# Kernel tuning notes

Hardware: AMD Instinct MI355X
Metric: run time of the kernel (lower is better)

Reference implementation:

```python
import jax, jax.numpy as jnp
import numpy as np

DIM = 4096
N_HEADS = 32
N_KV = 8
HEAD_DIM = DIM // N_HEADS  # 128
R = N_HEADS // N_KV        # 4 query heads per kv head
B, T = 2, 2048


def setup_inputs() -> dict:
    key = jax.random.key(0)
    kx, kq, kkv, ko = jax.random.split(key, 4)
    scale = 0.02
    return {
        "x": jax.random.normal(kx, (B, T, DIM), dtype=jnp.float32),
        "Wq": jax.random.normal(kq, (DIM, DIM), dtype=jnp.float32) * scale,
        "Wkv": jax.random.normal(kkv, (2 * N_KV * HEAD_DIM, DIM), dtype=jnp.float32) * scale,
        "Wo": jax.random.normal(ko, (DIM, DIM), dtype=jnp.float32) * scale,
    }


def reference(x, Wq, Wkv, Wo):
    Bs, Ts, C = x.shape
    # projections (torch Linear: y = x @ W.T)
    q = (x @ Wq.T).reshape(Bs, Ts, N_HEADS, HEAD_DIM).transpose(0, 2, 1, 3)  # [B,H,T,hd]
    kv = x @ Wkv.T                                                            # [B,T,2*KV*hd]
    k, v = jnp.split(kv, 2, axis=-1)
    k = k.reshape(Bs, Ts, N_KV, HEAD_DIM).transpose(0, 2, 1, 3)  # [B,KV,T,hd]
    v = v.reshape(Bs, Ts, N_KV, HEAD_DIM).transpose(0, 2, 1, 3)  # [B,KV,T,hd]
    # grouped query heads: head h = g*R + r matches repeat_interleave(R, dim=1)
    qg = q.reshape(Bs, N_KV, R, Ts, HEAD_DIM)                    # [B,KV,R,T,hd]
    inv_scale = 1.0 / np.sqrt(HEAD_DIM).astype(np.float32)
    scores = jnp.einsum("bgrtd,bgsd->bgrts", qg, k) * inv_scale  # [B,KV,R,T,T]
    causal = jnp.tril(jnp.ones((Ts, Ts), dtype=bool))
    scores = jnp.where(causal, scores, jnp.finfo(scores.dtype).min)
    attn = jax.nn.softmax(scores, axis=-1)
    o = jnp.einsum("bgrts,bgsd->bgrtd", attn, v)                 # [B,KV,R,T,hd]
    o = o.reshape(Bs, N_HEADS, Ts, HEAD_DIM).transpose(0, 2, 1, 3).reshape(Bs, Ts, C)
    return o @ Wo.T
```

## Files before the change

### kernel.cpp

```cpp
#include <hip/hip_runtime.h>
#include <hip/hip_bf16.h>
#include <cstdint>
#include <type_traits>

#define DIM    4096
#define NHEADS 32
#define NKVH   8
#define HD     128
#define BATCH  2
#define SEQ    2048
#define MROWS  (BATCH*SEQ)
#define NQKV   6144
#define KOFF   4096
#define VOFF   5120

typedef __attribute__((ext_vector_type(8))) __bf16 bf16x8;
typedef __attribute__((ext_vector_type(4))) float  f32x4;

#define QSCALE 0.1275174338f

__device__ __forceinline__ void gl_lds16(const __bf16* g, __bf16* l) {
    __builtin_amdgcn_global_load_lds(
        (const __attribute__((address_space(1))) void*)g,
        (__attribute__((address_space(3))) void*)l, 16, 0, 0);
}

__global__ void cast_f32_bf16(const float* __restrict__ s, __bf16* __restrict__ d, int n8) {
    int i = blockIdx.x * 256 + threadIdx.x;
    if (i >= n8) return;
    float4 a = ((const float4*)s)[2*i];
    float4 b = ((const float4*)s)[2*i+1];
    bf16x8 v;
    v[0]=(__bf16)a.x; v[1]=(__bf16)a.y; v[2]=(__bf16)a.z; v[3]=(__bf16)a.w;
    v[4]=(__bf16)b.x; v[5]=(__bf16)b.y; v[6]=(__bf16)b.z; v[7]=(__bf16)b.w;
    ((bf16x8*)d)[i] = v;
}

template<typename OutT>
__global__ __launch_bounds__(256)
void gemm_bt(const __bf16* __restrict__ A, const __bf16* __restrict__ Bm,
             OutT* __restrict__ C, int M, int N, int K,
             float scale, int scale_cols)
{
    __shared__ __bf16 As[128*64];
    __shared__ __bf16 Bs[128*64];
    const int tid  = threadIdx.x;
    const int lane = tid & 63;
    const int w    = tid >> 6;
    const int quad = lane >> 4;
    const int l16  = lane & 15;
    const int m0   = blockIdx.y * 128;
    const int n0   = blockIdx.x * 128;
    const int wm   = (w & 1) * 64;
    const int wn   = (w >> 1) * 64;

    const __bf16* Ab = A  + (size_t)m0 * K;
    const __bf16* Bb = Bm + (size_t)n0 * K;

    f32x4 acc[4][4] = {};

    for (int k0 = 0; k0 < K; k0 += 64) {
        __syncthreads();
        #pragma unroll
        for (int r = 0; r < 4; ++r) {
            int chunk = r*256 + tid;
            int row = chunk >> 3, c8 = chunk & 7;
            int c8s = c8 ^ (row & 7);
            gl_lds16(Ab + (size_t)row*K + k0 + c8s*8, As + chunk*8);
            gl_lds16(Bb + (size_t)row*K + k0 + c8s*8, Bs + chunk*8);
        }
        __syncthreads();
        #pragma unroll
        for (int t = 0; t < 2; ++t) {
            bf16x8 af[4], bfr[4];
            #pragma unroll
            for (int i = 0; i < 4; ++i) {
                int row = wm + i*16 + l16;
                int cc  = (t*4 + quad) ^ (row & 7);
                af[i] = *(const bf16x8*)(As + row*64 + cc*8);
            }
            #pragma unroll
            for (int j = 0; j < 4; ++j) {
                int row = wn + j*16 + l16;
                int cc  = (t*4 + quad) ^ (row & 7);
                bfr[j] = *(const bf16x8*)(Bs + row*64 + cc*8);
            }
            #pragma unroll
            for (int i = 0; i < 4; ++i)
                #pragma unroll
                for (int j = 0; j < 4; ++j)
                    acc[i][j] = __builtin_amdgcn_mfma_f32_16x16x32_bf16(af[i], bfr[j], acc[i][j], 0,0,0);
        }
    }

    #pragma unroll
    for (int i = 0; i < 4; ++i) {
        #pragma unroll
        for (int j = 0; j < 4; ++j) {
            int col = n0 + wn + j*16 + l16;
            float sc = (col < scale_cols) ? scale : 1.0f;
            #pragma unroll
            for (int r = 0; r < 4; ++r) {
                int row = m0 + wm + i*16 + quad*4 + r;
                float v = acc[i][j][r] * sc;
                if constexpr (std::is_same<OutT, float>::value)
                    C[(size_t)row * N + col] = v;
                else
                    C[(size_t)row * N + col] = (__bf16)v;
            }
        }
    }
}

__global__ void transpose_v(const __bf16* __restrict__ qkv, __bf16* __restrict__ vt) {
    int idx  = blockIdx.x * 256 + threadIdx.x;
    int s8   = idx & 255;
    int rest = idx >> 8;
    int d    = rest & (HD-1);
    int bg   = rest >> 7;
    int b    = bg >> 3;
    int g    = bg & 7;
    int s0   = s8 * 8;
    const __bf16* src = qkv + (size_t)(b*SEQ + s0)*NQKV + VOFF + g*HD + d;
    bf16x8 v;
    #pragma unroll
    for (int u = 0; u < 8; ++u) v[u] = src[(size_t)u*NQKV];
    *(bf16x8*)(vt + (size_t)rest*SEQ + s0) = v;
}

#define PSTR 72

__global__ __launch_bounds__(256)
void flash_attn(const __bf16* __restrict__ qkv, const __bf16* __restrict__ vt,
                __bf16* __restrict__ O)
{
    __shared__ __bf16 Ks[64*128];
    __shared__ __bf16 Vts[128*64];
    __shared__ __bf16 Ps[64*PSTR];

    const int qt = (gridDim.x - 1) - blockIdx.x;
    const int bh = blockIdx.y;
    const int b  = bh >> 5;
    const int h  = bh & 31;
    const int g  = h >> 2;
    const int q0 = qt * 64;

    const int tid  = threadIdx.x;
    const int lane = tid & 63;
    const int w    = tid >> 6;
    const int quad = lane >> 4;
    const int l16  = lane & 15;

    const __bf16* Qb  = qkv + (size_t)(b*SEQ + q0)*NQKV + h*HD;
    const __bf16* Kb  = qkv + (size_t)(b*SEQ)*NQKV + KOFF + g*HD;
    const __bf16* Vtb = vt  + (size_t)((b*NKVH + g)*HD)*SEQ;

    bf16x8 qf[4];
    #pragma unroll
    for (int t = 0; t < 4; ++t)
        qf[t] = *(const bf16x8*)(Qb + (size_t)(w*16 + l16)*NQKV + t*32 + quad*8);

    f32x4 o_acc[8] = {};
    float m_i[4], l_i[4];
    #pragma unroll
    for (int r = 0; r < 4; ++r) { m_i[r] = -1e30f; l_i[r] = 0.f; }

    const int nkt = qt + 1;
    for (int kt = 0; kt < nkt; ++kt) {
        const int s0 = kt * 64;
        __syncthreads();
        #pragma unroll
        for (int r = 0; r < 4; ++r) {
            int c = r*256 + tid;
            { int row = c >> 4, c16 = c & 15;
              int c16s = c16 ^ (row & 7);
              gl_lds16(Kb + (size_t)(s0 + row)*NQKV + c16s*8, Ks + c*8); }
            { int dd = c >> 3, c8 = c & 7;
              int c8s = c8 ^ (dd & 7);
              gl_lds16(Vtb + (size_t)dd*SEQ + s0 + c8s*8, Vts + c*8); }
        }
        __syncthreads();

        f32x4 s_acc[4] = {};
        #pragma unroll
        for (int t = 0; t < 4; ++t) {
            #pragma unroll
            for (int j = 0; j < 4; ++j) {
                int row = j*16 + l16;
                int cc  = (t*4 + quad) ^ (row & 7);
                bf16x8 bk = *(const bf16x8*)(Ks + row*128 + cc*8);
                s_acc[j] = __builtin_amdgcn_mfma_f32_16x16x32_bf16(qf[t], bk, s_acc[j], 0,0,0);
            }
        }

        if (kt == nkt - 1) {
            #pragma unroll
            for (int j = 0; j < 4; ++j) {
                int col = s0 + j*16 + l16;
                #pragma unroll
                for (int r = 0; r < 4; ++r) {
                    int qrow = q0 + w*16 + quad*4 + r;
                    if (col > qrow) s_acc[j][r] = -1e30f;
                }
            }
        }

        float mnew[4], alpha[4], psum[4];
        #pragma unroll
        for (int r = 0; r < 4; ++r) {
            float pm = fmaxf(fmaxf(s_acc[0][r], s_acc[1][r]), fmaxf(s_acc[2][r], s_acc[3][r]));
            pm = fmaxf(pm, __shfl_xor(pm, 1));
            pm = fmaxf(pm, __shfl_xor(pm, 2));
            pm = fmaxf(pm, __shfl_xor(pm, 4));
            pm = fmaxf(pm, __shfl_xor(pm, 8));
            mnew[r]  = fmaxf(m_i[r], pm);
            alpha[r] = exp2f(m_i[r] - mnew[r]);
            m_i[r]   = mnew[r];
            psum[r]  = 0.f;
        }
        #pragma unroll
        for (int j = 0; j < 4; ++j) {
            #pragma unroll
            for (int r = 0; r < 4; ++r) {
                float p = exp2f(s_acc[j][r] - mnew[r]);
                psum[r] += p;
                Ps[(w*16 + quad*4 + r)*PSTR + j*16 + l16] = (__bf16)p;
            }
        }
        #pragma unroll
        for (int r = 0; r < 4; ++r) {
            float ps = psum[r];
            ps += __shfl_xor(ps, 1);
            ps += __shfl_xor(ps, 2);
            ps += __shfl_xor(ps, 4);
            ps += __shfl_xor(ps, 8);
            l_i[r] = l_i[r]*alpha[r] + ps;
        }
        #pragma unroll
        for (int jt = 0; jt < 8; ++jt)
            #pragma unroll
            for (int r = 0; r < 4; ++r)
                o_acc[jt][r] *= alpha[r];

        #pragma unroll
        for (int t = 0; t < 2; ++t) {
            bf16x8 ap = *(const bf16x8*)(Ps + (w*16 + l16)*PSTR + t*32 + quad*8);
            #pragma unroll
            for (int jt = 0; jt < 8; ++jt) {
                int row = jt*16 + l16;
                int cc  = (t*4 + quad) ^ (row & 7);
                bf16x8 bv = *(const bf16x8*)(Vts + row*64 + cc*8);
                o_acc[jt] = __builtin_amdgcn_mfma_f32_16x16x32_bf16(ap, bv, o_acc[jt], 0,0,0);
            }
        }
    }

    float invl[4];
    #pragma unroll
    for (int r = 0; r < 4; ++r) invl[r] = 1.0f / l_i[r];
    #pragma unroll
    for (int jt = 0; jt < 8; ++jt) {
        #pragma unroll
        for (int r = 0; r < 4; ++r) {
            int row = q0 + w*16 + quad*4 + r;
            int col = h*HD + jt*16 + l16;
            O[(size_t)(b*SEQ + row)*DIM + col] = (__bf16)(o_acc[jt][r] * invl[r]);
        }
    }
}

extern "C" void kernel_launch(void* const* d_in, const int* in_sizes, int n_in,
                              void* d_out, int out_size, void* d_ws, size_t ws_size,
                              hipStream_t stream) {
    const float* x   = (const float*)d_in[0];
    const float* Wq  = (const float*)d_in[1];
    const float* Wkv = (const float*)d_in[2];
    const float* Wo  = (const float*)d_in[3];

    const size_t OFF_XB   = 0;
    const size_t OFF_WQKV = 33554432;
    const size_t OFF_WO   = 83886080;
    const size_t OFF_QKV  = 117440512;
    const size_t OFF_VT   = 167772160;
    const size_t OFF_OB   = 176160768;
    const size_t NEEDED   = 209715200;
    if (ws_size < NEEDED) return;

    char* ws = (char*)d_ws;
    __bf16* xb   = (__bf16*)(ws + OFF_XB);
    __bf16* wqkv = (__bf16*)(ws + OFF_WQKV);
    __bf16* wo   = (__bf16*)(ws + OFF_WO);
    __bf16* qkv  = (__bf16*)(ws + OFF_QKV);
    __bf16* vt   = (__bf16*)(ws + OFF_VT);
    __bf16* ob   = (__bf16*)(ws + OFF_OB);

    cast_f32_bf16<<<16777216/8/256, 256, 0, stream>>>(x,   xb,              16777216/8);
    cast_f32_bf16<<<16777216/8/256, 256, 0, stream>>>(Wq,  wqkv,            16777216/8);
    cast_f32_bf16<<< 8388608/8/256, 256, 0, stream>>>(Wkv, wqkv + 16777216,  8388608/8);
    cast_f32_bf16<<<16777216/8/256, 256, 0, stream>>>(Wo,  wo,              16777216/8);

    gemm_bt<__bf16><<<dim3(NQKV/128, MROWS/128), 256, 0, stream>>>(
        xb, wqkv, qkv, MROWS, NQKV, DIM, QSCALE, DIM);

    transpose_v<<<524288/256, 256, 0, stream>>>(qkv, vt);

    flash_attn<<<dim3(SEQ/64, BATCH*NHEADS), 256, 0, stream>>>(qkv, vt, ob);

    gemm_bt<float><<<dim3(DIM/128, MROWS/128), 256, 0, stream>>>(
        ob, wo, (float*)d_out, MROWS, DIM, DIM, 1.0f, 0);
}
```

Measured before the change: 967.3 us.

## Transpose S tile so softmax row reductions are mostly in-thread

The QK^T MFMA operands are swapped so each lane holds scores for a single query row across 16 key columns. The row max and sum then need only two cross-lane shuffles instead of four per row, and alpha and 1/l are broadcast with __shfl. The P tile is written as packed bf16x4 into an XOR-swizzled 64-wide LDS buffer instead of scalar stores into a padded one, and the launch bounds now request 4 blocks per CU. Risks are extra shuffles for the alpha broadcast and register pressure from the occupancy hint.

```diff
diff --git a/kernel.cpp b/kernel.cpp
--- a/kernel.cpp
+++ b/kernel.cpp
@@ -15,6 +15,7 @@
 #define VOFF   5120
 
 typedef __attribute__((ext_vector_type(8))) __bf16 bf16x8;
+typedef __attribute__((ext_vector_type(4))) __bf16 bf16x4;
 typedef __attribute__((ext_vector_type(4))) float  f32x4;
 
 #define QSCALE 0.1275174338f
@@ -128,15 +129,13 @@
     *(bf16x8*)(vt + (size_t)rest*SEQ + s0) = v;
 }
 
-#define PSTR 72
-
-__global__ __launch_bounds__(256)
+__global__ __launch_bounds__(256, 4)
 void flash_attn(const __bf16* __restrict__ qkv, const __bf16* __restrict__ vt,
                 __bf16* __restrict__ O)
 {
     __shared__ __bf16 Ks[64*128];
     __shared__ __bf16 Vts[128*64];
-    __shared__ __bf16 Ps[64*PSTR];
+    __shared__ __bf16 Ps[64*64];
 
     const int qt = (gridDim.x - 1) - blockIdx.x;
     const int bh = blockIdx.y;
@@ -150,6 +149,7 @@
     const int w    = tid >> 6;
     const int quad = lane >> 4;
     const int l16  = lane & 15;
+    const int psw  = (l16 & 7) << 1;
 
     const __bf16* Qb  = qkv + (size_t)(b*SEQ + q0)*NQKV + h*HD;
     const __bf16* Kb  = qkv + (size_t)(b*SEQ)*NQKV + KOFF + g*HD;
@@ -161,9 +161,8 @@
         qf[t] = *(const bf16x8*)(Qb + (size_t)(w*16 + l16)*NQKV + t*32 + quad*8);
 
     f32x4 o_acc[8] = {};
-    float m_i[4], l_i[4];
-    #pragma unroll
-    for (int r = 0; r < 4; ++r) { m_i[r] = -1e30f; l_i[r] = 0.f; }
+    float m_i = -1e30f, l_i = 0.f;
+    const int myrow = q0 + w*16 + l16;
 
     const int nkt = qt + 1;
     for (int kt = 0; kt < nkt; ++kt) {
@@ -189,62 +188,60 @@
                 int row = j*16 + l16;
                 int cc  = (t*4 + quad) ^ (row & 7);
                 bf16x8 bk = *(const bf16x8*)(Ks + row*128 + cc*8);
-                s_acc[j] = __builtin_amdgcn_mfma_f32_16x16x32_bf16(qf[t], bk, s_acc[j], 0,0,0);
+                s_acc[j] = __builtin_amdgcn_mfma_f32_16x16x32_bf16(bk, qf[t], s_acc[j], 0,0,0);
             }
         }
 
         if (kt == nkt - 1) {
             #pragma unroll
-            for (int j = 0; j < 4; ++j) {
-                int col = s0 + j*16 + l16;
+            for (int j = 0; j < 4; ++j)
                 #pragma unroll
-                for (int r = 0; r < 4; ++r) {
-                    int qrow = q0 + w*16 + quad*4 + r;
-                    if (col > qrow) s_acc[j][r] = -1e30f;
-                }
-            }
-        }
-
-        float mnew[4], alpha[4], psum[4];
-        #pragma unroll
-        for (int r = 0; r < 4; ++r) {
-            float pm = fmaxf(fmaxf(s_acc[0][r], s_acc[1][r]), fmaxf(s_acc[2][r], s_acc[3][r]));
-            pm = fmaxf(pm, __shfl_xor(pm, 1));
-            pm = fmaxf(pm, __shfl_xor(pm, 2));
-            pm = fmaxf(pm, __shfl_xor(pm, 4));
-            pm = fmaxf(pm, __shfl_xor(pm, 8));
-            mnew[r]  = fmaxf(m_i[r], pm);
-            alpha[r] = exp2f(m_i[r] - mnew[r]);
-            m_i[r]   = mnew[r];
-            psum[r]  = 0.f;
-        }
+                for (int r = 0; r < 4; ++r)
+                    if (s0 + j*16 + quad*4 + r > myrow) s_acc[j][r] = -1e30f;
+        }
+
+        float pm = s_acc[0][0];
+        #pragma unroll
+        for (int j = 0; j < 4; ++j)
+            #pragma unroll
+            for (int r = 0; r < 4; ++r)
+                pm = fmaxf(pm, s_acc[j][r]);
+        pm = fmaxf(pm, __shfl_xor(pm, 16));
+        pm = fmaxf(pm, __shfl_xor(pm, 32));
+        float mnew  = fmaxf(m_i, pm);
+        float alpha = exp2f(m_i - mnew);
+        m_i = mnew;
+
+        float psum = 0.f;
         #pragma unroll
         for (int j = 0; j < 4; ++j) {
+            bf16x4 pv;
             #pragma unroll
             for (int r = 0; r < 4; ++r) {
-                float p = exp2f(s_acc[j][r] - mnew[r]);
-                psum[r] += p;
-                Ps[(w*16 + quad*4 + r)*PSTR + j*16 + l16] = (__bf16)p;
-            }
-        }
-        #pragma unroll
-        for (int r = 0; r < 4; ++r) {
-            float ps = psum[r];
-            ps += __shfl_xor(ps, 1);
-            ps += __shfl_xor(ps, 2);
-            ps += __shfl_xor(ps, 4);
-            ps += __shfl_xor(ps, 8);
-            l_i[r] = l_i[r]*alpha[r] + ps;
-        }
+                float p = exp2f(s_acc[j][r] - mnew);
+                psum += p;
+                pv[r] = (__bf16)p;
+            }
+            int cs = (j*4 + quad) ^ psw;
+            *(bf16x4*)(Ps + (w*16 + l16)*64 + cs*4) = pv;
+        }
+        psum += __shfl_xor(psum, 16);
+        psum += __shfl_xor(psum, 32);
+        l_i = l_i*alpha + psum;
+
+        float av[4];
+        #pragma unroll
+        for (int r = 0; r < 4; ++r) av[r] = __shfl(alpha, quad*4 + r);
         #pragma unroll
         for (int jt = 0; jt < 8; ++jt)
             #pragma unroll
             for (int r = 0; r < 4; ++r)
-                o_acc[jt][r] *= alpha[r];
+                o_acc[jt][r] *= av[r];
 
         #pragma unroll
         for (int t = 0; t < 2; ++t) {
-            bf16x8 ap = *(const bf16x8*)(Ps + (w*16 + l16)*PSTR + t*32 + quad*8);
+            int cs = (t*8 + quad*2) ^ psw;
+            bf16x8 ap = *(const bf16x8*)(Ps + (w*16 + l16)*64 + cs*4);
             #pragma unroll
             for (int jt = 0; jt < 8; ++jt) {
                 int row = jt*16 + l16;
@@ -255,16 +252,17 @@
         }
     }
 
-    float invl[4];
-    #pragma unroll
-    for (int r = 0; r < 4; ++r) invl[r] = 1.0f / l_i[r];
+    float inv = 1.0f / l_i;
+    float ivr[4];
+    #pragma unroll
+    for (int r = 0; r < 4; ++r) ivr[r] = __shfl(inv, quad*4 + r);
     #pragma unroll
     for (int jt = 0; jt < 8; ++jt) {
         #pragma unroll
         for (int r = 0; r < 4; ++r) {
             int row = q0 + w*16 + quad*4 + r;
             int col = h*HD + jt*16 + l16;
-            O[(size_t)(b*SEQ + row)*DIM + col] = (__bf16)(o_acc[jt][r] * invl[r]);
+            O[(size_t)(b*SEQ + row)*DIM + col] = (__bf16)(o_acc[jt][r] * ivr[r]);
         }
     }
 }
```

Measured after the change: 850.6 us. 1.14x faster.
